# Kernel tuning notes

Measured on AMD Instinct MI355X. Metric: run time of the kernel, lower is better.

Reference implementation:

```python
import jax, jax.numpy as jnp
import numpy as np

GRID_SIZE = 5
SPLINE_ORDER = 3
GRID_RANGE = (-1.0, 1.0)


def b_splines(x, grid, spline_order=SPLINE_ORDER):
    # x: [B, in], grid: [G] with G = grid_size + 2*spline_order + 1
    x = x[..., None]                      # [B, in, 1]
    g = grid[None, None, :]               # [1, 1, G]
    bases = ((x >= g[..., :-1]) & (x < g[..., 1:])).astype(x.dtype)  # [B, in, G-1]
    for k in range(1, spline_order + 1):
        left = (x - g[..., :-(k + 1)]) / (g[..., k:-1] - g[..., :-(k + 1)]) * bases[..., :-1]
        right = (g[..., k + 1:] - x) / (g[..., k + 1:] - g[..., 1:-k]) * bases[..., 1:]
        bases = left + right
    return bases                          # [B, in, grid_size + spline_order]


def setup_inputs() -> dict:
    key = jax.random.key(0)
    k1, k2, k3, k4 = jax.random.split(key, 4)
    B, IN, OUT = 32768, 256, 256
    n_coef = GRID_SIZE + SPLINE_ORDER  # 8
    h = (GRID_RANGE[1] - GRID_RANGE[0]) / GRID_SIZE
    grid = jnp.arange(-SPLINE_ORDER, GRID_SIZE + SPLINE_ORDER + 1, dtype=jnp.float32) * h + GRID_RANGE[0]  # [12]
    x = jax.random.normal(k1, (B, IN), dtype=jnp.float32)
    base_weight = jax.random.normal(k2, (OUT, IN), dtype=jnp.float32) * np.sqrt(2.0 / IN)
    spline_weight = jax.random.normal(k3, (OUT, IN, n_coef), dtype=jnp.float32) * (0.1 / GRID_SIZE)
    spline_scaler = jax.random.normal(k4, (OUT, IN), dtype=jnp.float32) * np.sqrt(2.0 / IN)
    return {"x": x, "base_weight": base_weight, "spline_weight": spline_weight,
            "spline_scaler": spline_scaler, "grid": grid}


def reference(x, base_weight, spline_weight, spline_scaler, grid):
    B = x.shape[0]
    out_features = base_weight.shape[0]
    # base branch: silu(x) @ base_weight^T
    base_out = jnp.matmul(jax.nn.silu(x), base_weight.T)  # [B, out]
    # spline branch
    bases = b_splines(x, grid)                             # [B, in, n_coef]
    scaled_w = spline_weight * spline_scaler[..., None]    # [out, in, n_coef]
    spline_out = jnp.matmul(bases.reshape(B, -1), scaled_w.reshape(out_features, -1).T)
    return base_out + spline_out
```

## Files before the change

kernel.cpp:

```cpp
#include <hip/hip_runtime.h>
#include <stdint.h>


#define IN_F 256
#define OUT_F 256
#define KDIM 2304
#define BK 64
#define NCHUNK (KDIM / BK)

typedef float f32x4 __attribute__((ext_vector_type(4)));
typedef short bf16x8 __attribute__((ext_vector_type(8)));

__device__ __forceinline__ uint32_t f2bf(float f) {
    union { float f; uint32_t u; } c; c.f = f;
    uint32_t u = c.u;
    return (u + 0x7FFFu + ((u >> 16) & 1u)) >> 16;
}

__device__ __forceinline__ float silu_f(float v) {
    return v / (1.0f + __expf(-v));
}

__device__ __forceinline__ void block_sync_lds() {
    __builtin_amdgcn_sched_barrier(0);
    asm volatile("s_waitcnt lgkmcnt(0)" ::: "memory");
    __builtin_amdgcn_sched_barrier(0);
    __builtin_amdgcn_s_barrier();
    __builtin_amdgcn_sched_barrier(0);
}

__device__ __forceinline__ uint4 basis16(float xx) {
    float u = __builtin_fmaf(xx, 2.5f, 5.5f);
    float jf = floorf(u);
    float t = u - jf;
    int j0 = (int)jf;
    float t2 = t * t, t3 = t2 * t;
    float p3 = t3 * (1.0f / 6.0f);
    float p2 = __builtin_fmaf(t3, -0.5f,
               __builtin_fmaf(t2, 0.5f, __builtin_fmaf(t, 0.5f, 1.0f / 6.0f)));
    float p1 = __builtin_fmaf(t3, 0.5f, __builtin_fmaf(t2, -1.0f, 2.0f / 3.0f));
    float omt = 1.0f - t;
    float p0 = omt * omt * omt * (1.0f / 6.0f);
    uint32_t b0 = f2bf(p0), b1 = f2bf(p1), b2 = f2bf(p2), b3 = f2bf(p3);
    const int s0 = j0 - 3;
    int ds = s0 >> 1;
    if ((unsigned)j0 > 10u) ds = 9;
    const bool odd = (s0 & 1) != 0;
    uint32_t v0 = odd ? (b0 << 16) : (b0 | (b1 << 16));
    uint32_t v1 = odd ? (b1 | (b2 << 16)) : (b2 | (b3 << 16));
    uint32_t v2 = odd ? b3 : 0u;
    uint4 r;
    r.x = (ds == 0) ? v0 : (ds == -1) ? v1 : (ds == -2) ? v2 : 0u;
    r.y = (ds == 1) ? v0 : (ds ==  0) ? v1 : (ds == -1) ? v2 : 0u;
    r.z = (ds == 2) ? v0 : (ds ==  1) ? v1 : (ds ==  0) ? v2 : 0u;
    r.w = (ds == 3) ? v0 : (ds ==  2) ? v1 : (ds ==  1) ? v2 : 0u;
    return r;
}

__device__ __forceinline__ size_t wcf_addr(int col, int k) {
    const int kc = k >> 6, kkh = (k >> 5) & 1, q = (k >> 3) & 3, e = k & 7;
    return ((size_t)((kc * 2 + kkh) * 16 + (col >> 4))) * 512 +
           (size_t)(q * 16 + (col & 15)) * 8 + e;
}

__global__ void build_w(const float* __restrict__ bw, const float* __restrict__ sw,
                        const float* __restrict__ ss, unsigned short* __restrict__ WcF) {
    const int o = blockIdx.x;
    const int i = threadIdx.x;
    WcF[wcf_addr(o, i)] = (unsigned short)f2bf(bw[o * IN_F + i]);
    const float scal = ss[o * IN_F + i];
    const float4* swv = reinterpret_cast<const float4*>(sw + (size_t)(o * IN_F + i) * 8);
    float4 s0 = swv[0], s1 = swv[1];
    uint4 wv;
    wv.x = f2bf(s0.x * scal) | (f2bf(s0.y * scal) << 16);
    wv.y = f2bf(s0.z * scal) | (f2bf(s0.w * scal) << 16);
    wv.z = f2bf(s1.x * scal) | (f2bf(s1.y * scal) << 16);
    wv.w = f2bf(s1.z * scal) | (f2bf(s1.w * scal) << 16);
    *reinterpret_cast<uint4*>(WcF + wcf_addr(o, IN_F + i * 8)) = wv;
}

__launch_bounds__(512, 2)
__global__ void kan_fused(const float* __restrict__ x, const unsigned short* __restrict__ WcF,
                          float* __restrict__ out) {
    __shared__ __align__(16) unsigned short As[2][128 * 64];

    const int bid = blockIdx.x;
    const int row0 = bid * 128;
    const int tid = threadIdx.x;
    const int lane = tid & 63;
    const int w = tid >> 6;
    const int wm = w >> 2;
    const int wn = w & 3;
    const int l15 = lane & 15;
    const int q = lane >> 4;

    const int erow = tid >> 2;
    const int qd   = tid & 3;

    f32x4 acc[4][4] = {};
    bf16x8 bE[8], bO[8];
    float4 xE[4], xO[4];

    const unsigned short* wbase = WcF + (size_t)lane * 8;

    auto load_b = [&](int kc, bf16x8* dst) {
#pragma unroll
        for (int nt = 0; nt < 4; ++nt)
#pragma unroll
            for (int kkh = 0; kkh < 2; ++kkh)
                dst[nt * 2 + kkh] = *reinterpret_cast<const bf16x8*>(
                    wbase + ((size_t)((kc * 2 + kkh) * 16 + wn * 4 + nt)) * 512);
    };
    auto load_x = [&](int c, float4* xs) {
        if (c < 4) {
            const float* xp = x + (size_t)(row0 + erow) * IN_F + c * 64 + qd * 16;
            xs[0] = reinterpret_cast<const float4*>(xp)[0];
            xs[1] = reinterpret_cast<const float4*>(xp)[1];
            xs[2] = reinterpret_cast<const float4*>(xp)[2];
            xs[3] = reinterpret_cast<const float4*>(xp)[3];
        } else {
            const float* xp = x + (size_t)(row0 + erow) * IN_F + (c - 4) * 8 + qd * 2;
            float2 v = *reinterpret_cast<const float2*>(xp);
            xs[0].x = v.x; xs[0].y = v.y;
        }
    };
    auto expand = [&](int c, const float4* xs, uint4& w0, uint4& w1) {
        if (c < 4) {
            w0.x = f2bf(silu_f(xs[0].x)) | (f2bf(silu_f(xs[0].y)) << 16);
            w0.y = f2bf(silu_f(xs[0].z)) | (f2bf(silu_f(xs[0].w)) << 16);
            w0.z = f2bf(silu_f(xs[1].x)) | (f2bf(silu_f(xs[1].y)) << 16);
            w0.w = f2bf(silu_f(xs[1].z)) | (f2bf(silu_f(xs[1].w)) << 16);
            w1.x = f2bf(silu_f(xs[2].x)) | (f2bf(silu_f(xs[2].y)) << 16);
            w1.y = f2bf(silu_f(xs[2].z)) | (f2bf(silu_f(xs[2].w)) << 16);
            w1.z = f2bf(silu_f(xs[3].x)) | (f2bf(silu_f(xs[3].y)) << 16);
            w1.w = f2bf(silu_f(xs[3].z)) | (f2bf(silu_f(xs[3].w)) << 16);
        } else {
            w0 = basis16(xs[0].x);
            w1 = basis16(xs[0].y);
        }
    };
    auto write_a = [&](int buf, const uint4& w0, const uint4& w1) {
        const int g0 = qd * 2;
        *reinterpret_cast<uint4*>(&As[buf][erow * 64 + ((g0 ^ (erow & 7)) << 3)]) = w0;
        *reinterpret_cast<uint4*>(&As[buf][erow * 64 + (((g0 + 1) ^ (erow & 7)) << 3)]) = w1;
    };
    auto mfma_chunk = [&](int cur, const bf16x8* bv) {
        bf16x8 af[2][4];
#pragma unroll
        for (int kkh = 0; kkh < 2; ++kkh) {
            const int g0 = kkh * 4 + q;
#pragma unroll
            for (int mt = 0; mt < 4; ++mt) {
                int r = wm * 64 + mt * 16 + l15;
                af[kkh][mt] = *reinterpret_cast<const bf16x8*>(
                    &As[cur][r * 64 + ((g0 ^ (r & 7)) << 3)]);
            }
        }
        __builtin_amdgcn_s_setprio(1);
#pragma unroll
        for (int kkh = 0; kkh < 2; ++kkh)
#pragma unroll
            for (int mt = 0; mt < 4; ++mt)
#pragma unroll
                for (int nt = 0; nt < 4; ++nt)
                    acc[mt][nt] = __builtin_amdgcn_mfma_f32_16x16x32_bf16(
                        af[kkh][mt], bv[nt * 2 + kkh], acc[mt][nt], 0, 0, 0);
        __builtin_amdgcn_s_setprio(0);
    };

    load_x(0, xE);
    load_x(1, xO);
    load_b(0, bE);
    {
        uint4 wa, wb;
        expand(0, xE, wa, wb);
        write_a(0, wa, wb);
    }
    block_sync_lds();

    for (int kc = 0; kc < NCHUNK; kc += 2) {
        {
            uint4 wa, wb;
            if (kc + 1 < NCHUNK) load_b(kc + 1, bO);
            if (kc + 2 < NCHUNK) load_x(kc + 2, xE);
            if (kc + 1 < NCHUNK) expand(kc + 1, xO, wa, wb);
            mfma_chunk(0, bE);
            if (kc + 1 < NCHUNK) write_a(1, wa, wb);
            block_sync_lds();
        }
        {
            uint4 wa, wb;
            if (kc + 2 < NCHUNK) load_b(kc + 2, bE);
            if (kc + 3 < NCHUNK) load_x(kc + 3, xO);
            if (kc + 2 < NCHUNK) expand(kc + 2, xE, wa, wb);
            mfma_chunk(1, bO);
            if (kc + 2 < NCHUNK) write_a(0, wa, wb);
            block_sync_lds();
        }
    }

#pragma unroll
    for (int mt = 0; mt < 4; ++mt) {
        int row = row0 + wm * 64 + mt * 16 + q * 4;
#pragma unroll
        for (int nt = 0; nt < 4; ++nt) {
            int col = wn * 64 + nt * 16 + l15;
#pragma unroll
            for (int r = 0; r < 4; ++r)
                out[(size_t)(row + r) * OUT_F + col] = acc[mt][nt][r];
        }
    }
}

extern "C" void kernel_launch(void* const* d_in, const int* in_sizes, int n_in,
                              void* d_out, int out_size, void* d_ws, size_t ws_size,
                              hipStream_t stream) {
    const float* x  = (const float*)d_in[0];
    const float* bw = (const float*)d_in[1];
    const float* sw = (const float*)d_in[2];
    const float* ss = (const float*)d_in[3];
    unsigned short* WcF = (unsigned short*)d_ws;

    build_w<<<dim3(OUT_F), dim3(IN_F), 0, stream>>>(bw, sw, ss, WcF);

    const int B_ROWS = in_sizes[0] / IN_F;
    kan_fused<<<dim3(B_ROWS / 128), dim3(512), 0, stream>>>(
        x, WcF, (float*)d_out);
}
```

Measured before the change: 138.1 us.

## Deepen A-tile pipeline to four LDS buffers with warp-staggered expand/MFMA ordering

Grows the shared A buffer from two to four chunks so two K-chunks are expanded and consumed per barrier, which halves the number of block syncs. Half the warps expand the spline bases before their MFMAs and the other half after, so VALU and MFMA work from different waves can overlap. Float-to-bf16 packing now uses the hardware v_cvt_pk_bf16_f32 instruction instead of manual integer rounding. A-fragment loads are interleaved with the MFMAs. The costs are doubled LDS use (64KB per block, which may affect the 2-blocks-per-CU occupancy), a hard-coded loop schedule tied to 36 chunks, and higher register pressure from the extra prefetched x values.

```diff
diff --git a/kernel.cpp b/kernel.cpp
--- a/kernel.cpp
+++ b/kernel.cpp
@@ -15,6 +15,12 @@
     union { float f; uint32_t u; } c; c.f = f;
     uint32_t u = c.u;
     return (u + 0x7FFFu + ((u >> 16) & 1u)) >> 16;
+}
+
+__device__ __forceinline__ uint32_t cvtpk(float lo, float hi) {
+    uint32_t r;
+    asm("v_cvt_pk_bf16_f32 %0, %1, %2" : "=v"(r) : "v"(lo), "v"(hi));
+    return r;
 }
 
 __device__ __forceinline__ float silu_f(float v) {
@@ -41,14 +47,13 @@
     float p1 = __builtin_fmaf(t3, 0.5f, __builtin_fmaf(t2, -1.0f, 2.0f / 3.0f));
     float omt = 1.0f - t;
     float p0 = omt * omt * omt * (1.0f / 6.0f);
-    uint32_t b0 = f2bf(p0), b1 = f2bf(p1), b2 = f2bf(p2), b3 = f2bf(p3);
     const int s0 = j0 - 3;
     int ds = s0 >> 1;
     if ((unsigned)j0 > 10u) ds = 9;
     const bool odd = (s0 & 1) != 0;
-    uint32_t v0 = odd ? (b0 << 16) : (b0 | (b1 << 16));
-    uint32_t v1 = odd ? (b1 | (b2 << 16)) : (b2 | (b3 << 16));
-    uint32_t v2 = odd ? b3 : 0u;
+    uint32_t v0 = cvtpk(odd ? 0.0f : p0, odd ? p0 : p1);
+    uint32_t v1 = cvtpk(odd ? p1 : p2, odd ? p2 : p3);
+    uint32_t v2 = odd ? cvtpk(p3, 0.0f) : 0u;
     uint4 r;
     r.x = (ds == 0) ? v0 : (ds == -1) ? v1 : (ds == -2) ? v2 : 0u;
     r.y = (ds == 1) ? v0 : (ds ==  0) ? v1 : (ds == -1) ? v2 : 0u;
@@ -82,7 +87,7 @@
 __launch_bounds__(512, 2)
 __global__ void kan_fused(const float* __restrict__ x, const unsigned short* __restrict__ WcF,
                           float* __restrict__ out) {
-    __shared__ __align__(16) unsigned short As[2][128 * 64];
+    __shared__ __align__(16) unsigned short As[4][128 * 64];
 
     const int bid = blockIdx.x;
     const int row0 = bid * 128;
@@ -99,7 +104,7 @@
 
     f32x4 acc[4][4] = {};
     bf16x8 bE[8], bO[8];
-    float4 xE[4], xO[4];
+    float2 x0, x1, x2, x3;
 
     const unsigned short* wbase = WcF + (size_t)lane * 8;
 
@@ -111,93 +116,130 @@
                 dst[nt * 2 + kkh] = *reinterpret_cast<const bf16x8*>(
                     wbase + ((size_t)((kc * 2 + kkh) * 16 + wn * 4 + nt)) * 512);
     };
-    auto load_x = [&](int c, float4* xs) {
-        if (c < 4) {
-            const float* xp = x + (size_t)(row0 + erow) * IN_F + c * 64 + qd * 16;
-            xs[0] = reinterpret_cast<const float4*>(xp)[0];
-            xs[1] = reinterpret_cast<const float4*>(xp)[1];
-            xs[2] = reinterpret_cast<const float4*>(xp)[2];
-            xs[3] = reinterpret_cast<const float4*>(xp)[3];
-        } else {
-            const float* xp = x + (size_t)(row0 + erow) * IN_F + (c - 4) * 8 + qd * 2;
-            float2 v = *reinterpret_cast<const float2*>(xp);
-            xs[0].x = v.x; xs[0].y = v.y;
-        }
-    };
-    auto expand = [&](int c, const float4* xs, uint4& w0, uint4& w1) {
-        if (c < 4) {
-            w0.x = f2bf(silu_f(xs[0].x)) | (f2bf(silu_f(xs[0].y)) << 16);
-            w0.y = f2bf(silu_f(xs[0].z)) | (f2bf(silu_f(xs[0].w)) << 16);
-            w0.z = f2bf(silu_f(xs[1].x)) | (f2bf(silu_f(xs[1].y)) << 16);
-            w0.w = f2bf(silu_f(xs[1].z)) | (f2bf(silu_f(xs[1].w)) << 16);
-            w1.x = f2bf(silu_f(xs[2].x)) | (f2bf(silu_f(xs[2].y)) << 16);
-            w1.y = f2bf(silu_f(xs[2].z)) | (f2bf(silu_f(xs[2].w)) << 16);
-            w1.z = f2bf(silu_f(xs[3].x)) | (f2bf(silu_f(xs[3].y)) << 16);
-            w1.w = f2bf(silu_f(xs[3].z)) | (f2bf(silu_f(xs[3].w)) << 16);
-        } else {
-            w0 = basis16(xs[0].x);
-            w1 = basis16(xs[0].y);
-        }
-    };
-    auto write_a = [&](int buf, const uint4& w0, const uint4& w1) {
+    auto load_x_silu = [&](int c, float4* xs4) {
+        const float* xp = x + (size_t)(row0 + erow) * IN_F + c * 64 + qd * 16;
+#pragma unroll
+        for (int i = 0; i < 4; ++i)
+            xs4[i] = reinterpret_cast<const float4*>(xp)[i];
+    };
+    auto load_x_bas = [&](int c, float2& v) {
+        v = *reinterpret_cast<const float2*>(
+            x + (size_t)(row0 + erow) * IN_F + (c - 4) * 8 + qd * 2);
+    };
+    auto expand_silu = [&](const float4* xs4, uint4& w0, uint4& w1) {
+        w0.x = cvtpk(silu_f(xs4[0].x), silu_f(xs4[0].y));
+        w0.y = cvtpk(silu_f(xs4[0].z), silu_f(xs4[0].w));
+        w0.z = cvtpk(silu_f(xs4[1].x), silu_f(xs4[1].y));
+        w0.w = cvtpk(silu_f(xs4[1].z), silu_f(xs4[1].w));
+        w1.x = cvtpk(silu_f(xs4[2].x), silu_f(xs4[2].y));
+        w1.y = cvtpk(silu_f(xs4[2].z), silu_f(xs4[2].w));
+        w1.z = cvtpk(silu_f(xs4[3].x), silu_f(xs4[3].y));
+        w1.w = cvtpk(silu_f(xs4[3].z), silu_f(xs4[3].w));
+    };
+    auto expand_bas = [&](float2 v, uint4& w0, uint4& w1) {
+        w0 = basis16(v.x);
+        w1 = basis16(v.y);
+    };
+    auto write_a = [&](unsigned short* Ab, const uint4& w0, const uint4& w1) {
         const int g0 = qd * 2;
-        *reinterpret_cast<uint4*>(&As[buf][erow * 64 + ((g0 ^ (erow & 7)) << 3)]) = w0;
-        *reinterpret_cast<uint4*>(&As[buf][erow * 64 + (((g0 + 1) ^ (erow & 7)) << 3)]) = w1;
-    };
-    auto mfma_chunk = [&](int cur, const bf16x8* bv) {
-        bf16x8 af[2][4];
+        *reinterpret_cast<uint4*>(Ab + erow * 64 + ((g0 ^ (erow & 7)) << 3)) = w0;
+        *reinterpret_cast<uint4*>(Ab + erow * 64 + (((g0 + 1) ^ (erow & 7)) << 3)) = w1;
+    };
+    auto mfma_chunk = [&](const unsigned short* Ab, const bf16x8* bv) {
 #pragma unroll
         for (int kkh = 0; kkh < 2; ++kkh) {
             const int g0 = kkh * 4 + q;
 #pragma unroll
             for (int mt = 0; mt < 4; ++mt) {
                 int r = wm * 64 + mt * 16 + l15;
-                af[kkh][mt] = *reinterpret_cast<const bf16x8*>(
-                    &As[cur][r * 64 + ((g0 ^ (r & 7)) << 3)]);
-            }
-        }
-        __builtin_amdgcn_s_setprio(1);
-#pragma unroll
-        for (int kkh = 0; kkh < 2; ++kkh)
-#pragma unroll
-            for (int mt = 0; mt < 4; ++mt)
+                bf16x8 a = *reinterpret_cast<const bf16x8*>(
+                    Ab + r * 64 + ((g0 ^ (r & 7)) << 3));
+                __builtin_amdgcn_s_setprio(1);
 #pragma unroll
                 for (int nt = 0; nt < 4; ++nt)
                     acc[mt][nt] = __builtin_amdgcn_mfma_f32_16x16x32_bf16(
-                        af[kkh][mt], bv[nt * 2 + kkh], acc[mt][nt], 0, 0, 0);
-        __builtin_amdgcn_s_setprio(0);
-    };
-
-    load_x(0, xE);
-    load_x(1, xO);
+                        a, bv[nt * 2 + kkh], acc[mt][nt], 0, 0, 0);
+                __builtin_amdgcn_s_setprio(0);
+            }
+        }
+    };
+
+    float4 xf2[4], xf3[4];
+    {
+        float4 t4[4]; uint4 a, b;
+        load_x_silu(0, t4); expand_silu(t4, a, b); write_a(&As[0][0], a, b);
+        load_x_silu(1, t4); expand_silu(t4, a, b); write_a(&As[1][0], a, b);
+    }
+    load_x_silu(2, xf2);
+    load_x_silu(3, xf3);
+    load_x_bas(4, x0);
+    load_x_bas(5, x1);
     load_b(0, bE);
+    block_sync_lds();
+
+    load_b(1, bO);
+    load_x_bas(6, x2);
+    load_x_bas(7, x3);
     {
-        uint4 wa, wb;
-        expand(0, xE, wa, wb);
-        write_a(0, wa, wb);
-    }
+        uint4 a2, b2, a3, b3;
+        expand_silu(xf2, a2, b2); expand_silu(xf3, a3, b3);
+        write_a(&As[2][0], a2, b2); write_a(&As[3][0], a3, b3);
+    }
+    mfma_chunk(&As[0][0], bE);
+    load_b(2, bE);
+    mfma_chunk(&As[1][0], bO);
     block_sync_lds();
 
-    for (int kc = 0; kc < NCHUNK; kc += 2) {
+    for (int t = 0; t < 8; ++t) {
         {
-            uint4 wa, wb;
-            if (kc + 1 < NCHUNK) load_b(kc + 1, bO);
-            if (kc + 2 < NCHUNK) load_x(kc + 2, xE);
-            if (kc + 1 < NCHUNK) expand(kc + 1, xO, wa, wb);
-            mfma_chunk(0, bE);
-            if (kc + 1 < NCHUNK) write_a(1, wa, wb);
+            const int kc = 4 * t + 2;
+            load_b(kc + 1, bO);
+            load_x_bas(kc + 4, x2);
+            load_x_bas(kc + 5, x3);
+            uint4 wa0, wb0, wa1, wb1;
+            if (w < 4) {
+                expand_bas(x0, wa0, wb0); expand_bas(x1, wa1, wb1);
+                write_a(&As[0][0], wa0, wb0); write_a(&As[1][0], wa1, wb1);
+                mfma_chunk(&As[2][0], bE);
+                load_b(kc + 2, bE);
+                mfma_chunk(&As[3][0], bO);
+            } else {
+                mfma_chunk(&As[2][0], bE);
+                load_b(kc + 2, bE);
+                mfma_chunk(&As[3][0], bO);
+                expand_bas(x0, wa0, wb0); expand_bas(x1, wa1, wb1);
+                write_a(&As[0][0], wa0, wb0); write_a(&As[1][0], wa1, wb1);
+            }
             block_sync_lds();
         }
         {
-            uint4 wa, wb;
-            if (kc + 2 < NCHUNK) load_b(kc + 2, bE);
-            if (kc + 3 < NCHUNK) load_x(kc + 3, xO);
-            if (kc + 2 < NCHUNK) expand(kc + 2, xE, wa, wb);
-            mfma_chunk(1, bO);
-            if (kc + 2 < NCHUNK) write_a(0, wa, wb);
+            const int kc2 = 4 * t + 4;
+            load_b(kc2 + 1, bO);
+            if (kc2 + 5 < NCHUNK) {
+                load_x_bas(kc2 + 4, x0);
+                load_x_bas(kc2 + 5, x1);
+            }
+            uint4 wa0, wb0, wa1, wb1;
+            if (w < 4) {
+                expand_bas(x2, wa0, wb0); expand_bas(x3, wa1, wb1);
+                write_a(&As[2][0], wa0, wb0); write_a(&As[3][0], wa1, wb1);
+                mfma_chunk(&As[0][0], bE);
+                load_b(kc2 + 2, bE);
+                mfma_chunk(&As[1][0], bO);
+            } else {
+                mfma_chunk(&As[0][0], bE);
+                load_b(kc2 + 2, bE);
+                mfma_chunk(&As[1][0], bO);
+                expand_bas(x2, wa0, wb0); expand_bas(x3, wa1, wb1);
+                write_a(&As[2][0], wa0, wb0); write_a(&As[3][0], wa1, wb1);
+            }
             block_sync_lds();
         }
     }
+
+    load_b(35, bO);
+    mfma_chunk(&As[2][0], bE);
+    mfma_chunk(&As[3][0], bO);
 
 #pragma unroll
     for (int mt = 0; mt < 4; ++mt) {
```

Result: no change. 137.1 us (-0.8%).
